# Kernel optimization log

Hardware: AMD Instinct MI355X
Metric: run time of the kernel (lower is better)

Reference implementation:

```python
import jax, jax.numpy as jnp
import numpy as np

LEARNING_RATE = 0.01


def setup_inputs() -> dict:
    key = jax.random.key(0)
    k1, k2 = jax.random.split(key)
    O, D = 512, 128  # output_dim, input_dim; batch must equal output_dim for the broadcast
    x = jax.random.normal(k1, (O, D), dtype=jnp.float32)
    weights = jax.random.normal(k2, (O, O, D), dtype=jnp.float32)
    return {"x": x, "weights": weights}


def reference(x, weights):
    # x: (B, D) with B == O; weights: (O, O, D)
    O = weights.shape[0]
    sigma = O / 2.0
    x = x.reshape(-1, weights.shape[-1])
    diff = weights - x[:, None, :]                      # (O, O, D)
    distances = jnp.sum(diff * diff, axis=-1)            # (O, O)
    winner = jnp.argmin(distances, axis=1)               # (O,)
    neighborhood = jnp.exp(-distances / (2.0 * sigma ** 2))  # (O, O)
    delta = LEARNING_RATE * neighborhood[..., None] * (x[:, None, :] - weights)  # (O, O, D)
    # torch: self.weights.data += torch.sum(delta, dim=0)  -> (O, D) broadcast over rows
    new_weights = weights + jnp.sum(delta, axis=0)        # (O, O, D)
    return winner, new_weights
```

## Files before the change

kernel.cpp:

```cpp
#include <hip/hip_runtime.h>
#include <stdint.h>

#define O_DIM 512
#define D_DIM 128
#define LR 0.01f
#define INV2SIG2 7.62939453125e-6f

#define LDS_ROWS 288
#define LDS_GRPS 18
#define HOLD_GRPS 14

typedef float f32x4 __attribute__((ext_vector_type(4)));

__global__ __launch_bounds__(512) void som_fused(
    const float* __restrict__ X,
    const float* __restrict__ W,
    float* __restrict__ dist,
    float* __restrict__ outW)
{
    const int j    = blockIdx.x;
    const int t    = threadIdx.x;
    const int wave = t >> 6;
    const int lane = t & 63;
    const int g    = lane >> 5;
    const int i32  = lane & 31;
    const int d0   = i32 * 4;
    const int rb   = wave * 2 + g;

    __shared__ float ldsW[LDS_ROWS * D_DIM];
    __shared__ float sacc[8][D_DIM];
    __shared__ float sS[D_DIM];

    f32x4 acc = {0.f, 0.f, 0.f, 0.f};

    #pragma unroll
    for (int bt = 0; bt < 3; ++bt) {
        f32x4 wv[6], xv[6];
        #pragma unroll
        for (int u = 0; u < 6; ++u) {
            const int b = (bt * 6 + u) * 16 + rb;
            wv[u] = *(const f32x4*)(W + ((size_t)b * O_DIM + j) * D_DIM + d0);
            xv[u] = *(const f32x4*)(X + (size_t)b * D_DIM + d0);
        }
        #pragma unroll
        for (int u = 0; u < 6; ++u) {
            const int b = (bt * 6 + u) * 16 + rb;
            const f32x4 dx = wv[u] - xv[u];
            float sum = dx.x * dx.x;
            sum = fmaf(dx.y, dx.y, sum);
            sum = fmaf(dx.z, dx.z, sum);
            sum = fmaf(dx.w, dx.w, sum);
            sum += __shfl_xor(sum, 1, 64);
            sum += __shfl_xor(sum, 2, 64);
            sum += __shfl_xor(sum, 4, 64);
            sum += __shfl_xor(sum, 8, 64);
            sum += __shfl_xor(sum, 16, 64);

            if (i32 == 0) dist[(size_t)b * O_DIM + j] = sum;

            const float c = LR * __expf(-sum * INV2SIG2);
            acc -= c * dx;

            *(f32x4*)(&ldsW[b * D_DIM + d0]) = wv[u];
        }
    }

    f32x4 whold[HOLD_GRPS];
    #pragma unroll
    for (int bt = 0; bt < 4; ++bt) {
        const int n = (bt < 3) ? 4 : 2;
        f32x4 xv[4];
        #pragma unroll
        for (int u = 0; u < 4; ++u) {
            if (u < n) {
                const int idx = bt * 4 + u;
                const int b = (LDS_GRPS + idx) * 16 + rb;
                whold[idx] = *(const f32x4*)(W + ((size_t)b * O_DIM + j) * D_DIM + d0);
                xv[u] = *(const f32x4*)(X + (size_t)b * D_DIM + d0);
            }
        }
        #pragma unroll
        for (int u = 0; u < 4; ++u) {
            if (u < n) {
                const int idx = bt * 4 + u;
                const int b = (LDS_GRPS + idx) * 16 + rb;
                const f32x4 dx = whold[idx] - xv[u];
                float sum = dx.x * dx.x;
                sum = fmaf(dx.y, dx.y, sum);
                sum = fmaf(dx.z, dx.z, sum);
                sum = fmaf(dx.w, dx.w, sum);
                sum += __shfl_xor(sum, 1, 64);
                sum += __shfl_xor(sum, 2, 64);
                sum += __shfl_xor(sum, 4, 64);
                sum += __shfl_xor(sum, 8, 64);
                sum += __shfl_xor(sum, 16, 64);

                if (i32 == 0) dist[(size_t)b * O_DIM + j] = sum;

                const float c = LR * __expf(-sum * INV2SIG2);
                acc -= c * dx;
            }
        }
    }

    acc.x += __shfl_xor(acc.x, 32, 64);
    acc.y += __shfl_xor(acc.y, 32, 64);
    acc.z += __shfl_xor(acc.z, 32, 64);
    acc.w += __shfl_xor(acc.w, 32, 64);

    if (lane < 32) *(f32x4*)(&sacc[wave][d0]) = acc;
    __syncthreads();
    if (t < D_DIM) {
        float v = sacc[0][t];
        #pragma unroll
        for (int w = 1; w < 8; ++w) v += sacc[w][t];
        sS[t] = v;
    }
    __syncthreads();
    const f32x4 s4 = *(const f32x4*)(sS + d0);

    #pragma unroll
    for (int idx = 0; idx < HOLD_GRPS; ++idx) {
        const int b = (LDS_GRPS + idx) * 16 + rb;
        __builtin_nontemporal_store(
            whold[idx] + s4, (f32x4*)(outW + ((size_t)b * O_DIM + j) * D_DIM + d0));
    }
    #pragma unroll 6
    for (int grp = 0; grp < LDS_GRPS; ++grp) {
        const int b = grp * 16 + rb;
        const f32x4 wv = *(const f32x4*)(&ldsW[b * D_DIM + d0]);
        __builtin_nontemporal_store(
            wv + s4, (f32x4*)(outW + ((size_t)b * O_DIM + j) * D_DIM + d0));
    }
}

__global__ __launch_bounds__(64) void som_argmin(
    const float* __restrict__ dist,
    float* __restrict__ out)
{
    const int b = blockIdx.x;
    const int lane = threadIdx.x;
    unsigned long long best = ~0ull;
    #pragma unroll
    for (int k = 0; k < 8; ++k) {
        const int jj = k * 64 + lane;
        const float s = dist[(size_t)b * O_DIM + jj];
        const unsigned long long key =
            ((unsigned long long)__float_as_uint(s) << 32) | (unsigned int)jj;
        best = key < best ? key : best;
    }
    #pragma unroll
    for (int m = 32; m >= 1; m >>= 1) {
        const unsigned long long o = __shfl_xor(best, m, 64);
        best = o < best ? o : best;
    }
    if (lane == 0) out[b] = (float)(unsigned int)(best & 0xFFFFFFFFull);
}


__global__ __launch_bounds__(256) void som_pass1_atomic(
    const float* __restrict__ X, const float* __restrict__ W,
    float* __restrict__ S, unsigned long long* __restrict__ wkey)
{
    const int j = blockIdx.x >> 2, chunk = blockIdx.x & 3;
    const int wave = threadIdx.x >> 6, lane = threadIdx.x & 63;
    const int d0 = lane * 2;
    float accx = 0.f, accy = 0.f;
    const int b_end = chunk * 128 + 128;
    for (int b = chunk * 128 + wave; b < b_end; b += 4) {
        const float2 w2 = *(const float2*)(W + ((size_t)b * O_DIM + j) * D_DIM + d0);
        const float2 x2 = *(const float2*)(X + (size_t)b * D_DIM + d0);
        const float dx = w2.x - x2.x, dy = w2.y - x2.y;
        float s = dx * dx + dy * dy;
        #pragma unroll
        for (int m = 32; m >= 1; m >>= 1) s += __shfl_xor(s, m, 64);
        if (lane == 0)
            atomicMin(&wkey[b], ((unsigned long long)__float_as_uint(s) << 32) | (unsigned)j);
        const float c = LR * __expf(-s * INV2SIG2);
        accx -= c * dx; accy -= c * dy;
    }
    __shared__ float sacc[D_DIM];
    if (threadIdx.x < D_DIM) sacc[threadIdx.x] = 0.f;
    __syncthreads();
    atomicAdd(&sacc[d0], accx); atomicAdd(&sacc[d0 + 1], accy);
    __syncthreads();
    if (threadIdx.x < D_DIM) atomicAdd(&S[(size_t)j * D_DIM + threadIdx.x], sacc[threadIdx.x]);
}

__global__ __launch_bounds__(256) void som_pass2_atomic(
    const float* __restrict__ W, const float* __restrict__ S,
    const unsigned long long* __restrict__ wkey, float* __restrict__ out)
{
    const size_t tid = (size_t)blockIdx.x * blockDim.x + threadIdx.x;
    if (tid < O_DIM) out[tid] = (float)(unsigned int)(wkey[tid] & 0xFFFFFFFFull);
    float* __restrict__ outW = out + O_DIM;
    const size_t total4 = (size_t)O_DIM * O_DIM * D_DIM / 4;
    const size_t stride = (size_t)gridDim.x * blockDim.x;
    for (size_t i = tid; i < total4; i += stride) {
        const size_t e = i * 4;
        const float4 w4 = *(const float4*)(W + e);
        const float4 s4 = *(const float4*)(S + (e & (size_t)(O_DIM * D_DIM - 1)));
        float4 o4 = {w4.x + s4.x, w4.y + s4.y, w4.z + s4.z, w4.w + s4.w};
        *(float4*)(outW + e) = o4;
    }
}

extern "C" void kernel_launch(void* const* d_in, const int* in_sizes, int n_in,
                              void* d_out, int out_size, void* d_ws, size_t ws_size,
                              hipStream_t stream)
{
    const float* X = (const float*)d_in[0];
    const float* W = (const float*)d_in[1];
    float* out = (float*)d_out;

    const size_t DIST_BYTES = (size_t)O_DIM * O_DIM * sizeof(float);

    if (ws_size >= DIST_BYTES) {
        float* dist = (float*)d_ws;
        som_fused <<<dim3(512), dim3(512), 0, stream>>>(X, W, dist, out + O_DIM);
        som_argmin<<<dim3(512), dim3(64),  0, stream>>>(dist, out);
    } else {
        float* S = (float*)d_ws;
        unsigned long long* wkey =
            (unsigned long long*)((char*)d_ws + (size_t)O_DIM * D_DIM * sizeof(float));
        hipMemsetAsync(S, 0, (size_t)O_DIM * D_DIM * sizeof(float), stream);
        hipMemsetAsync(wkey, 0xFF, (size_t)O_DIM * sizeof(unsigned long long), stream);
        som_pass1_atomic<<<dim3(2048), dim3(256), 0, stream>>>(X, W, S, wkey);
        som_pass2_atomic<<<dim3(2048), dim3(256), 0, stream>>>(W, S, wkey, out);
    }
}
```

Before: 54.75 us.

## Shrink LDS staging and re-read part of W from global to raise occupancy

Reduces the LDS row cache from 18 to 8 row groups and adds 10 row groups that are read once to compute distances and read again from global memory when writing the updated weights. The aim is a smaller shared memory footprint per block so more blocks can be resident per CU and memory latency is hidden better. In exchange, part of the weight tensor is read twice from global memory, increasing traffic unless caches catch the re-reads.

Measured after the change: 55.44 us. No clear change (+1.3%).

```diff
diff --git a/kernel.cpp b/kernel.cpp
--- a/kernel.cpp
+++ b/kernel.cpp
@@ -6,9 +6,9 @@
 #define LR 0.01f
 #define INV2SIG2 7.62939453125e-6f
 
-#define LDS_ROWS 288
-#define LDS_GRPS 18
+#define LDS_GRPS 8
 #define HOLD_GRPS 14
+#define RR_GRPS 10
 
 typedef float f32x4 __attribute__((ext_vector_type(4)));
 
@@ -27,24 +27,24 @@
     const int d0   = i32 * 4;
     const int rb   = wave * 2 + g;
 
-    __shared__ float ldsW[LDS_ROWS * D_DIM];
+    __shared__ float ldsW[LDS_GRPS * 16 * D_DIM];
     __shared__ float sacc[8][D_DIM];
     __shared__ float sS[D_DIM];
 
     f32x4 acc = {0.f, 0.f, 0.f, 0.f};
 
     #pragma unroll
-    for (int bt = 0; bt < 3; ++bt) {
-        f32x4 wv[6], xv[6];
-        #pragma unroll
-        for (int u = 0; u < 6; ++u) {
-            const int b = (bt * 6 + u) * 16 + rb;
+    for (int bt = 0; bt < 2; ++bt) {
+        f32x4 wv[4], xv[4];
+        #pragma unroll
+        for (int u = 0; u < 4; ++u) {
+            const int b = (bt * 4 + u) * 16 + rb;
             wv[u] = *(const f32x4*)(W + ((size_t)b * O_DIM + j) * D_DIM + d0);
             xv[u] = *(const f32x4*)(X + (size_t)b * D_DIM + d0);
         }
         #pragma unroll
-        for (int u = 0; u < 6; ++u) {
-            const int b = (bt * 6 + u) * 16 + rb;
+        for (int u = 0; u < 4; ++u) {
+            const int b = (bt * 4 + u) * 16 + rb;
             const f32x4 dx = wv[u] - xv[u];
             float sum = dx.x * dx.x;
             sum = fmaf(dx.y, dx.y, sum);
@@ -103,6 +103,36 @@
         }
     }
 
+    #pragma unroll
+    for (int bt = 0; bt < 2; ++bt) {
+        f32x4 wv[5], xv[5];
+        #pragma unroll
+        for (int u = 0; u < 5; ++u) {
+            const int b = (LDS_GRPS + HOLD_GRPS + bt * 5 + u) * 16 + rb;
+            wv[u] = *(const f32x4*)(W + ((size_t)b * O_DIM + j) * D_DIM + d0);
+            xv[u] = *(const f32x4*)(X + (size_t)b * D_DIM + d0);
+        }
+        #pragma unroll
+        for (int u = 0; u < 5; ++u) {
+            const int b = (LDS_GRPS + HOLD_GRPS + bt * 5 + u) * 16 + rb;
+            const f32x4 dx = wv[u] - xv[u];
+            float sum = dx.x * dx.x;
+            sum = fmaf(dx.y, dx.y, sum);
+            sum = fmaf(dx.z, dx.z, sum);
+            sum = fmaf(dx.w, dx.w, sum);
+            sum += __shfl_xor(sum, 1, 64);
+            sum += __shfl_xor(sum, 2, 64);
+            sum += __shfl_xor(sum, 4, 64);
+            sum += __shfl_xor(sum, 8, 64);
+            sum += __shfl_xor(sum, 16, 64);
+
+            if (i32 == 0) dist[(size_t)b * O_DIM + j] = sum;
+
+            const float c = LR * __expf(-sum * INV2SIG2);
+            acc -= c * dx;
+        }
+    }
+
     acc.x += __shfl_xor(acc.x, 32, 64);
     acc.y += __shfl_xor(acc.y, 32, 64);
     acc.z += __shfl_xor(acc.z, 32, 64);
@@ -125,12 +155,27 @@
         __builtin_nontemporal_store(
             whold[idx] + s4, (f32x4*)(outW + ((size_t)b * O_DIM + j) * D_DIM + d0));
     }
-    #pragma unroll 6
+    #pragma unroll 4
     for (int grp = 0; grp < LDS_GRPS; ++grp) {
         const int b = grp * 16 + rb;
         const f32x4 wv = *(const f32x4*)(&ldsW[b * D_DIM + d0]);
         __builtin_nontemporal_store(
             wv + s4, (f32x4*)(outW + ((size_t)b * O_DIM + j) * D_DIM + d0));
+    }
+    #pragma unroll
+    for (int bt = 0; bt < 2; ++bt) {
+        f32x4 wx[5];
+        #pragma unroll
+        for (int u = 0; u < 5; ++u) {
+            const int b = (LDS_GRPS + HOLD_GRPS + bt * 5 + u) * 16 + rb;
+            wx[u] = *(const f32x4*)(W + ((size_t)b * O_DIM + j) * D_DIM + d0);
+        }
+        #pragma unroll
+        for (int u = 0; u < 5; ++u) {
+            const int b = (LDS_GRPS + HOLD_GRPS + bt * 5 + u) * 16 + rb;
+            __builtin_nontemporal_store(
+                wx[u] + s4, (f32x4*)(outW + ((size_t)b * O_DIM + j) * D_DIM + d0));
+        }
     }
 }
 
```
